# Optimization experiments

Hardware: AMD Instinct MI355X
Metric: run time of the kernel (lower is better)

## Reference

```python
import jax, jax.numpy as jnp
import numpy as np

B, S, HID = 2, 2048, 2048
H, KVH, D = 32, 8, 64
G = H // KVH  # kv groups


def _rotate_half(x):
    x1, x2 = jnp.split(x, 2, axis=-1)
    return jnp.concatenate((-x2, x1), axis=-1)


def setup_inputs() -> dict:
    key = jax.random.key(0)
    ks = jax.random.split(key, 7)
    return {
        "hidden_states": jax.random.normal(ks[0], (B, S, HID), dtype=jnp.float32),
        "cos": jax.random.normal(ks[1], (B, S, D), dtype=jnp.float32),
        "sin": jax.random.normal(ks[2], (B, S, D), dtype=jnp.float32),
        "attention_mask": jnp.ones((B, S), dtype=bool),
        "Wq": jax.random.normal(ks[3], (HID, HID), dtype=jnp.float32) * 0.02,
        "Wk": jax.random.normal(ks[4], (KVH * D, HID), dtype=jnp.float32) * 0.02,
        "Wv": jax.random.normal(ks[5], (KVH * D, HID), dtype=jnp.float32) * 0.02,
        "Wo": jax.random.normal(ks[6], (HID, HID), dtype=jnp.float32) * 0.02,
    }


def reference(hidden_states, cos, sin, attention_mask, Wq, Wk, Wv, Wo):
    scaling = D ** (-0.5)
    # projections -> [B, heads, S, D]
    q = jnp.einsum('bsh,eh->bse', hidden_states, Wq).reshape(B, S, H, D).transpose(0, 2, 1, 3)
    k = jnp.einsum('bsh,eh->bse', hidden_states, Wk).reshape(B, S, KVH, D).transpose(0, 2, 1, 3)
    v = jnp.einsum('bsh,eh->bse', hidden_states, Wv).reshape(B, S, KVH, D).transpose(0, 2, 1, 3)
    # RoPE (cos/sin broadcast over head dim 1)
    c = cos[:, None, :, :]
    s = sin[:, None, :, :]
    q = q * c + _rotate_half(q) * s
    k = k * c + _rotate_half(k) * s
    # GQA: view q as [B, KVH, G, S, D]; avoid materializing expanded k/v
    qg = q.reshape(B, KVH, G, S, D)
    scores = jnp.einsum('bkgsd,bktd->bkgst', qg, k) * scaling  # [B,KVH,G,S,T]
    mask = attention_mask[:, None, None, None, :]  # [B,1,1,1,T]
    scores = jnp.where(mask, scores, -jnp.inf)
    attn = jax.nn.softmax(scores, axis=-1)
    out = jnp.einsum('bkgst,bktd->bkgsd', attn, v)  # [B,KVH,G,S,D]
    out = out.reshape(B, H, S, D).transpose(0, 2, 1, 3).reshape(B, S, H * D)
    return jnp.einsum('bse,he->bsh', out, Wo)
```

## Files before the change

kernel.cpp:

```cpp
#include <hip/hip_runtime.h>


typedef __attribute__((ext_vector_type(8))) short bf16x8;
typedef __attribute__((ext_vector_type(4))) float f32x4;

#define MFMA_BF16(a, b, c) __builtin_amdgcn_mfma_f32_16x16x32_bf16((a), (b), (c), 0, 0, 0)

#define QSCALE 0.1803368801111204f

static __device__ __forceinline__ unsigned short f2b(float f) {
  unsigned int u = __float_as_uint(f);
  return (unsigned short)((u + 0x7FFFu + ((u >> 16) & 1u)) >> 16);
}

typedef __attribute__((address_space(1))) void gvoid;
typedef __attribute__((address_space(3))) void svoid;
static __device__ __forceinline__ void gll16(const void* g, void* l) {
  __builtin_amdgcn_global_load_lds((gvoid*)g, (svoid*)l, 16, 0, 0);
}

__global__ __launch_bounds__(256) void cvt4(
    const float* __restrict__ s0, const float* __restrict__ s1,
    const float* __restrict__ s2, const float* __restrict__ s3,
    unsigned short* __restrict__ d0, unsigned short* __restrict__ d1,
    unsigned short* __restrict__ d2, unsigned short* __restrict__ d3) {
  int i = blockIdx.x * 256 + threadIdx.x;
  const float* s; unsigned short* d; int off;
  if (i < 2097152)      { s = s0; d = d0; off = i; }
  else if (i < 3145728) { s = s1; d = d1; off = i - 2097152; }
  else if (i < 3407872) { s = s2; d = d2; off = i - 3145728; }
  else                  { s = s3; d = d3; off = i - 3407872; }
  float4 f = ((const float4*)s)[off];
  ushort4 o;
  o.x = f2b(f.x); o.y = f2b(f.y); o.z = f2b(f.z); o.w = f2b(f.w);
  ((ushort4*)d)[off] = o;
}

__global__ __launch_bounds__(256) void cvt_f32_bf16(const float* __restrict__ src,
                                                    unsigned short* __restrict__ dst,
                                                    int n4) {
  int i = blockIdx.x * 256 + threadIdx.x;
  if (i < n4) {
    float4 f = ((const float4*)src)[i];
    ushort4 o;
    o.x = f2b(f.x); o.y = f2b(f.y); o.z = f2b(f.z); o.w = f2b(f.w);
    ((ushort4*)dst)[i] = o;
  }
}


__global__ __launch_bounds__(256) void gemm_qkv(
    const unsigned short* __restrict__ X,
    const unsigned short* __restrict__ W,
    const float* __restrict__ cosp,
    const float* __restrict__ sinp,
    unsigned short* __restrict__ Qo,
    unsigned short* __restrict__ Ko,
    unsigned short* __restrict__ Vto) {
  constexpr int K = 2048;
  __shared__ unsigned short As[2][4096];
  __shared__ unsigned short Bs[2][4096];

  const int tid = threadIdx.x;
  const int lane = tid & 63;
  const int w = tid >> 6;
  const int lane15 = lane & 15, quad = lane >> 4;
  const int wm = (w >> 1) * 64, wn = (w & 1) * 64;

  const int flat = blockIdx.y * 24 + blockIdx.x;
  const int grp = flat / 96, rem = flat % 96;
  const int m0 = (grp * 4 + (rem & 3)) * 128;
  const int n0 = (rem >> 2) * 128;

  f32x4 acc[4][4];
#pragma unroll
  for (int i = 0; i < 4; ++i)
#pragma unroll
    for (int j = 0; j < 4; ++j) acc[i][j] = (f32x4){0.f, 0.f, 0.f, 0.f};

  const int rl = lane >> 2;
  const int scol = (((lane & 3) ^ (rl & 3)) * 8);
  const unsigned short* Asrc0 = X + (size_t)(m0 + w * 32 + rl) * K + scol;
  const unsigned short* Asrc1 = X + (size_t)(m0 + w * 32 + 16 + rl) * K + scol;
  const unsigned short* Bsrc0 = W + (size_t)(n0 + w * 32 + rl) * K + scol;
  const unsigned short* Bsrc1 = W + (size_t)(n0 + w * 32 + 16 + rl) * K + scol;

  const int roff = 32 * lane15 + 8 * (quad ^ (lane15 & 3));
  const int abase = (w >> 1) * 2048, bbase = (w & 1) * 2048;

#define STAGE_Q(bf, k0)                          \
  do {                                           \
    gll16(Asrc0 + (k0), &As[bf][w * 1024]);      \
    gll16(Asrc1 + (k0), &As[bf][w * 1024 + 512]);\
    gll16(Bsrc0 + (k0), &Bs[bf][w * 1024]);      \
    gll16(Bsrc1 + (k0), &Bs[bf][w * 1024 + 512]);\
  } while (0)

  STAGE_Q(0, 0);
  int cur = 0;
  for (int i = 0; i < 64; ++i) {
    __syncthreads();
    if (i < 63) STAGE_Q(cur ^ 1, (i + 1) * 32);
    bf16x8 a[4], b[4];
#pragma unroll
    for (int mt = 0; mt < 4; ++mt)
      a[mt] = *(const bf16x8*)&As[cur][abase + mt * 512 + roff];
#pragma unroll
    for (int nt = 0; nt < 4; ++nt)
      b[nt] = *(const bf16x8*)&Bs[cur][bbase + nt * 512 + roff];
#pragma unroll
    for (int mt = 0; mt < 4; ++mt)
#pragma unroll
      for (int nt = 0; nt < 4; ++nt)
        acc[mt][nt] = MFMA_BF16(a[mt], b[nt], acc[mt][nt]);
    cur ^= 1;
  }
#undef STAGE_Q

#pragma unroll
  for (int mt = 0; mt < 4; ++mt) {
    const int mbase = m0 + wm + mt * 16 + quad * 4;
#pragma unroll
    for (int nt = 0; nt < 4; ++nt) {
      const int n = n0 + wn + nt * 16 + lane15;
      const int d = n & 63;
#pragma unroll
      for (int r = 0; r < 4; ++r) {
        const int mm = mbase + r;
        const int bb = mm >> 11;
        const int ss = mm & 2047;
        float v = acc[mt][nt][r];
        if (n < 2560) {
          const float partner = acc[mt][nt ^ 2][r];
          const float rot = ((d & 32) == 0) ? -partner : partner;
          v = v * cosp[(size_t)mm * 64 + d] + rot * sinp[(size_t)mm * 64 + d];
        }
        if (n < 2048) {
          const int hh = n >> 6;
          Qo[(((size_t)bb * 32 + hh) * 2048 + ss) * 64 + d] = f2b(v * QSCALE);
        } else if (n < 2560) {
          const int kvh = (n - 2048) >> 6;
          Ko[(((size_t)bb * 8 + kvh) * 2048 + ss) * 64 + d] = f2b(v);
        } else {
          const int kvh = (n - 2560) >> 6;
          Vto[(((size_t)bb * 8 + kvh) * 64 + d) * 2048 + ss] = f2b(v);
        }
      }
    }
  }
}

__global__ __launch_bounds__(256) void gemm_out(
    const unsigned short* __restrict__ A,
    const unsigned short* __restrict__ W,
    float* __restrict__ out) {
  constexpr int K = 2048;
  __shared__ unsigned short As[2][4096];
  __shared__ unsigned short Bs[2][4096];

  const int tid = threadIdx.x;
  const int lane = tid & 63;
  const int w = tid >> 6;
  const int lane15 = lane & 15, quad = lane >> 4;
  const int wm = (w >> 1) * 64, wn = (w & 1) * 64;

  const int flat = blockIdx.y * 16 + blockIdx.x;
  const int grp = flat / 64, rem = flat % 64;
  const int m0 = (grp * 4 + (rem & 3)) * 128;
  const int n0 = (rem >> 2) * 128;

  f32x4 acc[4][4];
#pragma unroll
  for (int i = 0; i < 4; ++i)
#pragma unroll
    for (int j = 0; j < 4; ++j) acc[i][j] = (f32x4){0.f, 0.f, 0.f, 0.f};

  const int rl = lane >> 2;
  const int scol = (((lane & 3) ^ (rl & 3)) * 8);
  const unsigned short* Asrc0 = A + (size_t)(m0 + w * 32 + rl) * K + scol;
  const unsigned short* Asrc1 = A + (size_t)(m0 + w * 32 + 16 + rl) * K + scol;
  const unsigned short* Bsrc0 = W + (size_t)(n0 + w * 32 + rl) * K + scol;
  const unsigned short* Bsrc1 = W + (size_t)(n0 + w * 32 + 16 + rl) * K + scol;

  const int roff = 32 * lane15 + 8 * (quad ^ (lane15 & 3));
  const int abase = (w >> 1) * 2048, bbase = (w & 1) * 2048;

#define STAGE_O(bf, k0)                          \
  do {                                           \
    gll16(Asrc0 + (k0), &As[bf][w * 1024]);      \
    gll16(Asrc1 + (k0), &As[bf][w * 1024 + 512]);\
    gll16(Bsrc0 + (k0), &Bs[bf][w * 1024]);      \
    gll16(Bsrc1 + (k0), &Bs[bf][w * 1024 + 512]);\
  } while (0)

  STAGE_O(0, 0);
  int cur = 0;
  for (int i = 0; i < 64; ++i) {
    __syncthreads();
    if (i < 63) STAGE_O(cur ^ 1, (i + 1) * 32);
    bf16x8 a[4], b[4];
#pragma unroll
    for (int mt = 0; mt < 4; ++mt)
      a[mt] = *(const bf16x8*)&As[cur][abase + mt * 512 + roff];
#pragma unroll
    for (int nt = 0; nt < 4; ++nt)
      b[nt] = *(const bf16x8*)&Bs[cur][bbase + nt * 512 + roff];
#pragma unroll
    for (int mt = 0; mt < 4; ++mt)
#pragma unroll
      for (int nt = 0; nt < 4; ++nt)
        acc[mt][nt] = MFMA_BF16(a[mt], b[nt], acc[mt][nt]);
    cur ^= 1;
  }
#undef STAGE_O

#pragma unroll
  for (int mt = 0; mt < 4; ++mt) {
    const int mbase = m0 + wm + mt * 16 + quad * 4;
#pragma unroll
    for (int nt = 0; nt < 4; ++nt) {
      const int n = n0 + wn + nt * 16 + lane15;
#pragma unroll
      for (int r = 0; r < 4; ++r)
        out[(size_t)(mbase + r) * 2048 + n] = acc[mt][nt][r];
    }
  }
}

__global__ __launch_bounds__(256) void attn(
    const unsigned short* __restrict__ Q,
    const unsigned short* __restrict__ Kg,
    const unsigned short* __restrict__ Vg,
    unsigned short* __restrict__ Ctx) {
  __shared__ unsigned short Ks[64 * 64];
  __shared__ unsigned short Vs[64 * 64];
  __shared__ unsigned short Ps[128 * 64];

  const int blk = blockIdx.x;
  const int qt = blk & 15;
  const int h = (blk >> 4) & 31;
  const int b = blk >> 9;
  const int kv = h >> 2;
  const int tid = threadIdx.x;
  const int lane = tid & 63;
  const int w = tid >> 6;
  const int lane15 = lane & 15, quad = lane >> 4;
  const int l7 = lane15 & 7;

  const short ONE = (short)0x3F80;
  const bf16x8 aone = (lane15 == 0)
      ? (bf16x8){ONE, ONE, ONE, ONE, ONE, ONE, ONE, ONE}
      : (bf16x8){0, 0, 0, 0, 0, 0, 0, 0};

  bf16x8 aq[2][2];
#pragma unroll
  for (int g = 0; g < 2; ++g) {
    const unsigned short* Qb =
        Q + (((size_t)b * 32 + h) * 2048 + qt * 128 + w * 32 + g * 16 + lane15) * 64;
    aq[g][0] = *(const bf16x8*)(Qb + quad * 8);
    aq[g][1] = *(const bf16x8*)(Qb + 32 + quad * 8);
  }

  const unsigned short* Kbase = Kg + ((size_t)b * 8 + kv) * 131072;
  const unsigned short* Vbase = Vg + ((size_t)b * 8 + kv) * 131072;

  f32x4 o[2][4], ol[2];
#pragma unroll
  for (int g = 0; g < 2; ++g) {
    ol[g] = (f32x4){0.f, 0.f, 0.f, 0.f};
#pragma unroll
    for (int mt = 0; mt < 4; ++mt) o[g][mt] = (f32x4){0.f, 0.f, 0.f, 0.f};
  }

  const int ur = tid >> 3;
  const int us = (tid & 7) * 8;
  const int sws = ur * 64 + 8 * ((tid & 7) ^ (ur & 7));

  uint4 kp0 = *(const uint4*)&Kbase[ur * 64 + us];
  uint4 kp1 = *(const uint4*)&Kbase[(ur + 32) * 64 + us];
  uint4 vp0 = *(const uint4*)&Vbase[(size_t)ur * 2048 + us];
  uint4 vp1 = *(const uint4*)&Vbase[(size_t)(ur + 32) * 2048 + us];

  const int prow0 = (w * 32 + lane15) * 64;
  const int prow1 = prow0 + 16 * 64;
  const int g0 = 8 * (quad ^ l7);

  for (int kt = 0; kt < 32; ++kt) {
    __syncthreads();
    *(uint4*)&Ks[sws] = kp0;
    *(uint4*)&Ks[sws + 32 * 64] = kp1;
    *(uint4*)&Vs[sws] = vp0;
    *(uint4*)&Vs[sws + 32 * 64] = vp1;
    const int kn = (kt + 1) & 31;
    kp0 = *(const uint4*)&Kbase[kn * 4096 + ur * 64 + us];
    kp1 = *(const uint4*)&Kbase[kn * 4096 + (ur + 32) * 64 + us];
    vp0 = *(const uint4*)&Vbase[(size_t)ur * 2048 + kn * 64 + us];
    vp1 = *(const uint4*)&Vbase[(size_t)(ur + 32) * 2048 + kn * 64 + us];
    __syncthreads();

#pragma unroll
    for (int nt = 0; nt < 4; ++nt) {
      const int krow = (nt * 16 + lane15) * 64;
      const bf16x8 k0f = *(const bf16x8*)&Ks[krow + g0];
      const bf16x8 k1f = *(const bf16x8*)&Ks[krow + (g0 ^ 32)];
#pragma unroll
      for (int g = 0; g < 2; ++g) {
        f32x4 c = (f32x4){0.f, 0.f, 0.f, 0.f};
        c = MFMA_BF16(k0f, aq[g][0], c);
        c = MFMA_BF16(k1f, aq[g][1], c);
        const unsigned u0 = __float_as_uint(__builtin_amdgcn_exp2f(c[0])) + 0x8000u;
        const unsigned u1 = __float_as_uint(__builtin_amdgcn_exp2f(c[1])) + 0x8000u;
        const unsigned u2 = __float_as_uint(__builtin_amdgcn_exp2f(c[2])) + 0x8000u;
        const unsigned u3 = __float_as_uint(__builtin_amdgcn_exp2f(c[3])) + 0x8000u;
        uint2 pk;
        pk.x = __builtin_amdgcn_perm(u1, u0, 0x07060302u);
        pk.y = __builtin_amdgcn_perm(u3, u2, 0x07060302u);
        const int pg = 8 * ((2 * nt + (quad >> 1)) ^ l7) + (quad & 1) * 4;
        *(uint2*)&Ps[(g ? prow1 : prow0) + pg] = pk;
      }
    }

#pragma unroll
    for (int f = 0; f < 2; ++f) {
      const bf16x8 bp0 = *(const bf16x8*)&Ps[prow0 + (g0 ^ (f * 32))];
      const bf16x8 bp1 = *(const bf16x8*)&Ps[prow1 + (g0 ^ (f * 32))];
      ol[0] = MFMA_BF16(aone, bp0, ol[0]);
      ol[1] = MFMA_BF16(aone, bp1, ol[1]);
#pragma unroll
      for (int mt = 0; mt < 4; ++mt) {
        const bf16x8 av = *(const bf16x8*)&Vs[(mt * 16 + lane15) * 64 + (g0 ^ (f * 32))];
        o[0][mt] = MFMA_BF16(av, bp0, o[0][mt]);
        o[1][mt] = MFMA_BF16(av, bp1, o[1][mt]);
      }
    }
  }

#pragma unroll
  for (int g = 0; g < 2; ++g) {
    const float ls = __shfl(ol[g][0], lane15, 64);
    const float inv = 1.f / ls;
    unsigned short* Cb =
        Ctx + ((size_t)b * 2048 + qt * 128 + w * 32 + g * 16 + lane15) * 2048 +
        h * 64 + quad * 4;
#pragma unroll
    for (int mt = 0; mt < 4; ++mt) {
      ushort4 st4;
      st4.x = f2b(o[g][mt][0] * inv);
      st4.y = f2b(o[g][mt][1] * inv);
      st4.z = f2b(o[g][mt][2] * inv);
      st4.w = f2b(o[g][mt][3] * inv);
      *(ushort4*)&Cb[mt * 16] = st4;
    }
  }
}

extern "C" void kernel_launch(void* const* d_in, const int* in_sizes, int n_in,
                              void* d_out, int out_size, void* d_ws, size_t ws_size,
                              hipStream_t stream) {
  const float* hs   = (const float*)d_in[0];
  const float* cosp = (const float*)d_in[1];
  const float* sinp = (const float*)d_in[2];
  const float* Wq = (const float*)d_in[4];
  const float* Wk = (const float*)d_in[5];
  const float* Wv = (const float*)d_in[6];
  const float* Wo = (const float*)d_in[7];
  float* out = (float*)d_out;
  unsigned short* ws = (unsigned short*)d_ws;

  unsigned short* Xbf  = ws;
  unsigned short* Ctx  = ws;
  unsigned short* Wqkv = ws + 8388608;
  unsigned short* Wob  = ws + 8388608;
  unsigned short* Qb   = ws + 14680064;
  unsigned short* Kb   = ws + 23068672;
  unsigned short* Vtb  = ws + 25165824;

  cvt4<<<14336, 256, 0, stream>>>(hs, Wq, Wk, Wv,
                                  Xbf, Wqkv, Wqkv + 4194304, Wqkv + 5242880);
  gemm_qkv<<<dim3(24, 32), 256, 0, stream>>>(Xbf, Wqkv, cosp, sinp, Qb, Kb, Vtb);
  cvt_f32_bf16<<<4096, 256, 0, stream>>>(Wo, Wob, 1048576);
  attn<<<1024, 256, 0, stream>>>(Qb, Kb, Vtb, Ctx);
  gemm_out<<<dim3(16, 32), 256, 0, stream>>>(Ctx, Wob, out);
}
```

Baseline: 343.4 us.

## Use 512-thread blocks with larger tiles and triple-buffered GEMM pipelines

Both projection GEMMs now run 8 waves per block on larger output tiles (256x256 for QKV, 256x128 for the output projection). Operand tiles are triple-buffered so loads run two k-steps ahead, with explicit vmcnt waits and a single barrier per step. MFMA sections run at raised wave priority. The aim is better data reuse per LDS load and hiding global-load latency; the cost is fewer blocks (192 and 256 on a 256-CU part), more LDS per block, and the removal of the earlier grouped block-swizzle ordering.

```diff
diff --git a/kernel.cpp b/kernel.cpp
--- a/kernel.cpp
+++ b/kernel.cpp
@@ -49,7 +49,7 @@
 }
 
 
-__global__ __launch_bounds__(256) void gemm_qkv(
+__global__ __launch_bounds__(512, 2) void gemm_qkv(
     const unsigned short* __restrict__ X,
     const unsigned short* __restrict__ W,
     const float* __restrict__ cosp,
@@ -58,80 +58,95 @@
     unsigned short* __restrict__ Ko,
     unsigned short* __restrict__ Vto) {
   constexpr int K = 2048;
-  __shared__ unsigned short As[2][4096];
-  __shared__ unsigned short Bs[2][4096];
+  __shared__ unsigned short As0[8192], As1[8192], As2[8192];
+  __shared__ unsigned short Bs0[8192], Bs1[8192], Bs2[8192];
 
   const int tid = threadIdx.x;
   const int lane = tid & 63;
   const int w = tid >> 6;
   const int lane15 = lane & 15, quad = lane >> 4;
-  const int wm = (w >> 1) * 64, wn = (w & 1) * 64;
-
-  const int flat = blockIdx.y * 24 + blockIdx.x;
-  const int grp = flat / 96, rem = flat % 96;
-  const int m0 = (grp * 4 + (rem & 3)) * 128;
-  const int n0 = (rem >> 2) * 128;
-
-  f32x4 acc[4][4];
-#pragma unroll
-  for (int i = 0; i < 4; ++i)
+  const int wm = w >> 2, wn = w & 3;
+
+  const int m0 = blockIdx.y * 256;
+  const int n0 = blockIdx.x * 256;
+
+  f32x4 acc[8][4];
+#pragma unroll
+  for (int i = 0; i < 8; ++i)
 #pragma unroll
     for (int j = 0; j < 4; ++j) acc[i][j] = (f32x4){0.f, 0.f, 0.f, 0.f};
 
   const int rl = lane >> 2;
   const int scol = (((lane & 3) ^ (rl & 3)) * 8);
   const unsigned short* Asrc0 = X + (size_t)(m0 + w * 32 + rl) * K + scol;
-  const unsigned short* Asrc1 = X + (size_t)(m0 + w * 32 + 16 + rl) * K + scol;
+  const unsigned short* Asrc1 = Asrc0 + 16 * K;
   const unsigned short* Bsrc0 = W + (size_t)(n0 + w * 32 + rl) * K + scol;
-  const unsigned short* Bsrc1 = W + (size_t)(n0 + w * 32 + 16 + rl) * K + scol;
+  const unsigned short* Bsrc1 = Bsrc0 + 16 * K;
 
   const int roff = 32 * lane15 + 8 * (quad ^ (lane15 & 3));
-  const int abase = (w >> 1) * 2048, bbase = (w & 1) * 2048;
-
-#define STAGE_Q(bf, k0)                          \
-  do {                                           \
-    gll16(Asrc0 + (k0), &As[bf][w * 1024]);      \
-    gll16(Asrc1 + (k0), &As[bf][w * 1024 + 512]);\
-    gll16(Bsrc0 + (k0), &Bs[bf][w * 1024]);      \
-    gll16(Bsrc1 + (k0), &Bs[bf][w * 1024 + 512]);\
+  const int aoff = wm * 4096 + roff;
+  const int boff = wn * 2048 + roff;
+
+  unsigned short *Ac = As0, *An = As1, *Af = As2;
+  unsigned short *Bc = Bs0, *Bn = Bs1, *Bf = Bs2;
+
+#define STAGE_Q(Ad, Bd, k0)                \
+  do {                                     \
+    gll16(Asrc0 + (k0), &(Ad)[w * 1024]);  \
+    gll16(Asrc1 + (k0), &(Ad)[w * 1024 + 512]); \
+    gll16(Bsrc0 + (k0), &(Bd)[w * 1024]);  \
+    gll16(Bsrc1 + (k0), &(Bd)[w * 1024 + 512]); \
   } while (0)
 
-  STAGE_Q(0, 0);
-  int cur = 0;
-  for (int i = 0; i < 64; ++i) {
-    __syncthreads();
-    if (i < 63) STAGE_Q(cur ^ 1, (i + 1) * 32);
-    bf16x8 a[4], b[4];
-#pragma unroll
-    for (int mt = 0; mt < 4; ++mt)
-      a[mt] = *(const bf16x8*)&As[cur][abase + mt * 512 + roff];
-#pragma unroll
-    for (int nt = 0; nt < 4; ++nt)
-      b[nt] = *(const bf16x8*)&Bs[cur][bbase + nt * 512 + roff];
-#pragma unroll
-    for (int mt = 0; mt < 4; ++mt)
-#pragma unroll
-      for (int nt = 0; nt < 4; ++nt)
-        acc[mt][nt] = MFMA_BF16(a[mt], b[nt], acc[mt][nt]);
-    cur ^= 1;
+  STAGE_Q(As0, Bs0, 0);
+  STAGE_Q(As1, Bs1, 32);
+  asm volatile("s_waitcnt vmcnt(4)" ::: "memory");
+  __builtin_amdgcn_s_barrier();
+  asm volatile("" ::: "memory");
+
+  for (int t = 0; t < 64; ++t) {
+    if (t < 62) STAGE_Q(Af, Bf, (t + 2) * 32);
+
+    const bf16x8 b0 = *(const bf16x8*)&Bc[boff];
+    const bf16x8 b1 = *(const bf16x8*)&Bc[boff + 512];
+    const bf16x8 b2 = *(const bf16x8*)&Bc[boff + 1024];
+    const bf16x8 b3 = *(const bf16x8*)&Bc[boff + 1536];
+    __builtin_amdgcn_s_setprio(1);
+#pragma unroll
+    for (int mf = 0; mf < 8; ++mf) {
+      const bf16x8 a = *(const bf16x8*)&Ac[aoff + mf * 512];
+      acc[mf][0] = MFMA_BF16(a, b0, acc[mf][0]);
+      acc[mf][1] = MFMA_BF16(a, b1, acc[mf][1]);
+      acc[mf][2] = MFMA_BF16(a, b2, acc[mf][2]);
+      acc[mf][3] = MFMA_BF16(a, b3, acc[mf][3]);
+    }
+    __builtin_amdgcn_s_setprio(0);
+
+    if (t < 62)       asm volatile("s_waitcnt vmcnt(4)" ::: "memory");
+    else if (t == 62) asm volatile("s_waitcnt vmcnt(0)" ::: "memory");
+    __builtin_amdgcn_s_barrier();
+    asm volatile("" ::: "memory");
+
+    unsigned short* ta = Ac; Ac = An; An = Af; Af = ta;
+    unsigned short* tb = Bc; Bc = Bn; Bn = Bf; Bf = tb;
   }
 #undef STAGE_Q
 
 #pragma unroll
-  for (int mt = 0; mt < 4; ++mt) {
-    const int mbase = m0 + wm + mt * 16 + quad * 4;
-#pragma unroll
-    for (int nt = 0; nt < 4; ++nt) {
-      const int n = n0 + wn + nt * 16 + lane15;
+  for (int mf = 0; mf < 8; ++mf) {
+    const int mbase = m0 + wm * 128 + mf * 16 + quad * 4;
+#pragma unroll
+    for (int nf = 0; nf < 4; ++nf) {
+      const int n = n0 + wn * 64 + nf * 16 + lane15;
       const int d = n & 63;
 #pragma unroll
       for (int r = 0; r < 4; ++r) {
         const int mm = mbase + r;
         const int bb = mm >> 11;
         const int ss = mm & 2047;
-        float v = acc[mt][nt][r];
+        float v = acc[mf][nf][r];
         if (n < 2560) {
-          const float partner = acc[mt][nt ^ 2][r];
+          const float partner = acc[mf][nf ^ 2][r];
           const float rot = ((d & 32) == 0) ? -partner : partner;
           v = v * cosp[(size_t)mm * 64 + d] + rot * sinp[(size_t)mm * 64 + d];
         }
@@ -150,79 +165,88 @@
   }
 }
 
-__global__ __launch_bounds__(256) void gemm_out(
+__global__ __launch_bounds__(512, 2) void gemm_out(
     const unsigned short* __restrict__ A,
     const unsigned short* __restrict__ W,
     float* __restrict__ out) {
   constexpr int K = 2048;
-  __shared__ unsigned short As[2][4096];
-  __shared__ unsigned short Bs[2][4096];
+  __shared__ unsigned short As0[8192], As1[8192], As2[8192];
+  __shared__ unsigned short Bs0[4096], Bs1[4096], Bs2[4096];
 
   const int tid = threadIdx.x;
   const int lane = tid & 63;
   const int w = tid >> 6;
   const int lane15 = lane & 15, quad = lane >> 4;
-  const int wm = (w >> 1) * 64, wn = (w & 1) * 64;
-
-  const int flat = blockIdx.y * 16 + blockIdx.x;
-  const int grp = flat / 64, rem = flat % 64;
-  const int m0 = (grp * 4 + (rem & 3)) * 128;
-  const int n0 = (rem >> 2) * 128;
-
-  f32x4 acc[4][4];
-#pragma unroll
-  for (int i = 0; i < 4; ++i)
-#pragma unroll
-    for (int j = 0; j < 4; ++j) acc[i][j] = (f32x4){0.f, 0.f, 0.f, 0.f};
+  const int wm = w >> 2, wn = w & 3;
+
+  const int m0 = blockIdx.y * 256;
+  const int n0 = blockIdx.x * 128;
+
+  f32x4 acc[8][2];
+#pragma unroll
+  for (int i = 0; i < 8; ++i)
+#pragma unroll
+    for (int j = 0; j < 2; ++j) acc[i][j] = (f32x4){0.f, 0.f, 0.f, 0.f};
 
   const int rl = lane >> 2;
   const int scol = (((lane & 3) ^ (rl & 3)) * 8);
   const unsigned short* Asrc0 = A + (size_t)(m0 + w * 32 + rl) * K + scol;
-  const unsigned short* Asrc1 = A + (size_t)(m0 + w * 32 + 16 + rl) * K + scol;
-  const unsigned short* Bsrc0 = W + (size_t)(n0 + w * 32 + rl) * K + scol;
-  const unsigned short* Bsrc1 = W + (size_t)(n0 + w * 32 + 16 + rl) * K + scol;
+  const unsigned short* Asrc1 = Asrc0 + 16 * K;
+  const unsigned short* Bsrc0 = W + (size_t)(n0 + w * 16 + rl) * K + scol;
 
   const int roff = 32 * lane15 + 8 * (quad ^ (lane15 & 3));
-  const int abase = (w >> 1) * 2048, bbase = (w & 1) * 2048;
-
-#define STAGE_O(bf, k0)                          \
-  do {                                           \
-    gll16(Asrc0 + (k0), &As[bf][w * 1024]);      \
-    gll16(Asrc1 + (k0), &As[bf][w * 1024 + 512]);\
-    gll16(Bsrc0 + (k0), &Bs[bf][w * 1024]);      \
-    gll16(Bsrc1 + (k0), &Bs[bf][w * 1024 + 512]);\
+  const int aoff = wm * 4096 + roff;
+  const int boff = wn * 1024 + roff;
+
+  unsigned short *Ac = As0, *An = As1, *Af = As2;
+  unsigned short *Bc = Bs0, *Bn = Bs1, *Bf = Bs2;
+
+#define STAGE_O(Ad, Bd, k0)                \
+  do {                                     \
+    gll16(Asrc0 + (k0), &(Ad)[w * 1024]);  \
+    gll16(Asrc1 + (k0), &(Ad)[w * 1024 + 512]); \
+    gll16(Bsrc0 + (k0), &(Bd)[w * 512]);   \
   } while (0)
 
-  STAGE_O(0, 0);
-  int cur = 0;
-  for (int i = 0; i < 64; ++i) {
-    __syncthreads();
-    if (i < 63) STAGE_O(cur ^ 1, (i + 1) * 32);
-    bf16x8 a[4], b[4];
-#pragma unroll
-    for (int mt = 0; mt < 4; ++mt)
-      a[mt] = *(const bf16x8*)&As[cur][abase + mt * 512 + roff];
-#pragma unroll
-    for (int nt = 0; nt < 4; ++nt)
-      b[nt] = *(const bf16x8*)&Bs[cur][bbase + nt * 512 + roff];
-#pragma unroll
-    for (int mt = 0; mt < 4; ++mt)
-#pragma unroll
-      for (int nt = 0; nt < 4; ++nt)
-        acc[mt][nt] = MFMA_BF16(a[mt], b[nt], acc[mt][nt]);
-    cur ^= 1;
+  STAGE_O(As0, Bs0, 0);
+  STAGE_O(As1, Bs1, 32);
+  asm volatile("s_waitcnt vmcnt(3)" ::: "memory");
+  __builtin_amdgcn_s_barrier();
+  asm volatile("" ::: "memory");
+
+  for (int t = 0; t < 64; ++t) {
+    if (t < 62) STAGE_O(Af, Bf, (t + 2) * 32);
+
+    const bf16x8 b0 = *(const bf16x8*)&Bc[boff];
+    const bf16x8 b1 = *(const bf16x8*)&Bc[boff + 512];
+    __builtin_amdgcn_s_setprio(1);
+#pragma unroll
+    for (int mf = 0; mf < 8; ++mf) {
+      const bf16x8 a = *(const bf16x8*)&Ac[aoff + mf * 512];
+      acc[mf][0] = MFMA_BF16(a, b0, acc[mf][0]);
+      acc[mf][1] = MFMA_BF16(a, b1, acc[mf][1]);
+    }
+    __builtin_amdgcn_s_setprio(0);
+
+    if (t < 62)       asm volatile("s_waitcnt vmcnt(3)" ::: "memory");
+    else if (t == 62) asm volatile("s_waitcnt vmcnt(0)" ::: "memory");
+    __builtin_amdgcn_s_barrier();
+    asm volatile("" ::: "memory");
+
+    unsigned short* ta = Ac; Ac = An; An = Af; Af = ta;
+    unsigned short* tb = Bc; Bc = Bn; Bn = Bf; Bf = tb;
   }
 #undef STAGE_O
 
 #pragma unroll
-  for (int mt = 0; mt < 4; ++mt) {
-    const int mbase = m0 + wm + mt * 16 + quad * 4;
-#pragma unroll
-    for (int nt = 0; nt < 4; ++nt) {
-      const int n = n0 + wn + nt * 16 + lane15;
+  for (int mf = 0; mf < 8; ++mf) {
+    const int mbase = m0 + wm * 128 + mf * 16 + quad * 4;
+#pragma unroll
+    for (int nf = 0; nf < 2; ++nf) {
+      const int n = n0 + wn * 32 + nf * 16 + lane15;
 #pragma unroll
       for (int r = 0; r < 4; ++r)
-        out[(size_t)(mbase + r) * 2048 + n] = acc[mt][nt][r];
+        out[(size_t)(mbase + r) * 2048 + n] = acc[mf][nf][r];
     }
   }
 }
@@ -377,8 +401,8 @@
 
   cvt4<<<14336, 256, 0, stream>>>(hs, Wq, Wk, Wv,
                                   Xbf, Wqkv, Wqkv + 4194304, Wqkv + 5242880);
-  gemm_qkv<<<dim3(24, 32), 256, 0, stream>>>(Xbf, Wqkv, cosp, sinp, Qb, Kb, Vtb);
+  gemm_qkv<<<dim3(12, 16), 512, 0, stream>>>(Xbf, Wqkv, cosp, sinp, Qb, Kb, Vtb);
   cvt_f32_bf16<<<4096, 256, 0, stream>>>(Wo, Wob, 1048576);
   attn<<<1024, 256, 0, stream>>>(Qb, Kb, Vtb, Ctx);
-  gemm_out<<<dim3(16, 32), 256, 0, stream>>>(Ctx, Wob, out);
-}
+  gemm_out<<<dim3(16, 16), 512, 0, stream>>>(Ctx, Wob, out);
+}
```

After: 388.4 us. +13.1%, slower.
